# Performance work log

Hardware: AMD Instinct MI355X
Metric: run time of the kernel (lower is better)

Reference implementation:

```python
import jax, jax.numpy as jnp
import numpy as np

B, T, E, H = 2, 2048, 2048, 16
D = E // H  # head dim = 128
ROPE_BASE = 10000.0


def setup_inputs() -> dict:
    key = jax.random.key(0)
    ks = jax.random.split(key, 9)
    s = 1.0 / np.sqrt(E)
    return {
        "x": jax.random.normal(ks[0], (B, T, E), jnp.float32),
        "Wq": jax.random.normal(ks[1], (E, E), jnp.float32) * s,
        "bq": jax.random.normal(ks[2], (E,), jnp.float32) * s,
        "Wk": jax.random.normal(ks[3], (E, E), jnp.float32) * s,
        "bk": jax.random.normal(ks[4], (E,), jnp.float32) * s,
        "Wv": jax.random.normal(ks[5], (E, E), jnp.float32) * s,
        "bv": jax.random.normal(ks[6], (E,), jnp.float32) * s,
        "Wo": jax.random.normal(ks[7], (E, E), jnp.float32) * s,
        "bo": jax.random.normal(ks[8], (E,), jnp.float32) * s,
    }


def _rope(x):
    # x: [b, h, t, d]; positions are 1-indexed (m+1) as in the source
    t, d = x.shape[-2], x.shape[-1]
    j = jnp.arange(d // 2, dtype=x.dtype)
    thetas = ROPE_BASE ** (-2.0 * j / d)                  # [d/2]
    m = jnp.arange(1, t + 1, dtype=x.dtype)               # [t]
    ang = m[:, None] * thetas[None, :]                    # [t, d/2]
    C = jnp.concatenate([ang, ang], axis=-1)              # [t, d]
    x_rot = jnp.concatenate([-x[..., d // 2:], x[..., :d // 2]], axis=-1)
    return x * jnp.cos(C) + x_rot * jnp.sin(C)


def reference(x, Wq, bq, Wk, bk, Wv, bv, Wo, bo):
    b, t, e = x.shape
    # projections (nn.Linear: x @ W.T + b)
    def proj(W, bias):
        y = jnp.einsum('bte,fe->btf', x, W) + bias
        return y.reshape(b, t, H, D).transpose(0, 2, 1, 3)  # b h t d
    q = _rope(proj(Wq, bq))
    k = _rope(proj(Wk, bk))
    v = proj(Wv, bv)

    scale = jnp.sqrt(jnp.asarray(D, x.dtype))
    att = jnp.einsum('bhqd,bhkd->bhqk', q, k) / scale
    causal = jnp.tril(jnp.ones((t, t), bool))
    att = jnp.where(causal, att, -jnp.inf)
    att = jax.nn.softmax(att, axis=-1)
    y = jnp.einsum('bhqk,bhkd->bhqd', att, v)
    y = y.transpose(0, 2, 1, 3).reshape(b, t, e)
    y = jnp.einsum('bte,fe->btf', y, Wo) + bo
    return y
```

## Files before the change

### kernel.cpp

```cpp
#include <hip/hip_runtime.h>
#include <hip/hip_bf16.h>

typedef __bf16 bf16_t;
typedef __bf16 bf16x4 __attribute__((ext_vector_type(4)));
typedef __bf16 bf16x8 __attribute__((ext_vector_type(8)));
typedef float  f32x4  __attribute__((ext_vector_type(4)));

#define GLD_LDS16(gptr, lptr)                                                        \
    __builtin_amdgcn_global_load_lds((__attribute__((address_space(1))) void*)(gptr),\
                                     (__attribute__((address_space(3))) void*)(lptr),\
                                     16, 0, 0)

constexpr int Bc = 2, Tc = 2048, Ec = 2048, Hc = 16, Dc = 128;
constexpr int Mtok = Bc * Tc;

__device__ __forceinline__ bf16x8 cvt8(const float* p) {
    f32x4 a = *(const f32x4*)p;
    f32x4 b = *(const f32x4*)(p + 4);
    bf16x8 r;
    r[0] = (bf16_t)a[0]; r[1] = (bf16_t)a[1];
    r[2] = (bf16_t)a[2]; r[3] = (bf16_t)a[3];
    r[4] = (bf16_t)b[0]; r[5] = (bf16_t)b[1];
    r[6] = (bf16_t)b[2]; r[7] = (bf16_t)b[3];
    return r;
}

__global__ void convert_bf16(const float* __restrict__ src, bf16_t* __restrict__ dst) {
    size_t i = ((size_t)blockIdx.x * 256 + threadIdx.x) * 8;
    *(bf16x8*)&dst[i] = cvt8(src + i);
}

__global__ void convert_w(const float* __restrict__ Wq, const float* __restrict__ Wk,
                          const float* __restrict__ Wv, const float* __restrict__ Wo,
                          bf16_t* __restrict__ w4) {
    int blk = blockIdx.x;
    int wi  = blk >> 11;
    const float* src = (wi == 0) ? Wq : (wi == 1) ? Wk : (wi == 2) ? Wv : Wo;
    bf16_t* dst = w4 + (size_t)wi * Ec * Ec;
    size_t i = ((size_t)(blk & 2047) * 256 + threadIdx.x) * 8;
    *(bf16x8*)&dst[i] = cvt8(src + i);
}

__global__ __launch_bounds__(512, 2) void gemm_qkv_z(const bf16_t* __restrict__ A,
                                                     const bf16_t* __restrict__ w3,
                                                     const float* __restrict__ bq,
                                                     const float* __restrict__ bk,
                                                     const float* __restrict__ bv,
                                                     bf16_t* __restrict__ qo,
                                                     bf16_t* __restrict__ ko,
                                                     bf16_t* __restrict__ vto) {
    __shared__ __align__(16) bf16_t ldsA[3 * 8192];
    __shared__ __align__(16) bf16_t ldsB[3 * 12288];

    const int tid  = threadIdx.x;
    const int wave = tid >> 6;
    const int lane = tid & 63;
    const int g    = lane >> 4;
    const int n16  = lane & 15;
    const int wm   = wave >> 2;
    const int wn   = wave & 3;
    const int m0   = blockIdx.x * 256;
    const int n0   = blockIdx.y * 384;
    const int K    = Ec;

    const int sr   = tid >> 2;
    const int scol = (((tid & 3) ^ ((tid >> 3) & 3)) << 3);
    const bf16_t* srcA = A  + (size_t)(m0 + sr) * K + scol;
    const bf16_t* srcB = w3 + (size_t)(n0 + sr) * K + scol;
    const int dwave = wave * 512;

    const int fsw = (n16 >> 1) & 3;

    constexpr int NT = Ec / 32;

#define STG_A2(jj, buf)                                                         \
    do { if ((jj) < NT) {                                                       \
        const bf16_t* _s = srcA + (jj) * 32;                                    \
        bf16_t* _d = &ldsA[(buf) * 8192 + dwave];                               \
        GLD_LDS16(_s, _d);                                                      \
        GLD_LDS16(_s + (size_t)128 * K, _d + 4096);                             \
    } } while (0)
#define STG_B1(jj, buf)                                                         \
    do { if ((jj) < NT) {                                                       \
        GLD_LDS16(srcB + (jj) * 32, &ldsB[(buf) * 12288 + dwave]);              \
    } } while (0)
#define STG_B2(jj, buf)                                                         \
    do { if ((jj) < NT) {                                                       \
        const bf16_t* _s = srcB + (jj) * 32;                                    \
        bf16_t* _d = &ldsB[(buf) * 12288 + dwave];                              \
        GLD_LDS16(_s + (size_t)128 * K, _d + 4096);                             \
        GLD_LDS16(_s + (size_t)256 * K, _d + 8192);                             \
    } } while (0)

    f32x4 acc[8][6] = {};
    bf16x8 af[4], af2[4], bfr[6];

    STG_A2(0, 0); STG_B1(0, 0); STG_B2(0, 0);
    STG_A2(1, 1); STG_B1(1, 1); STG_B2(1, 1);
    asm volatile("s_waitcnt vmcnt(5)" ::: "memory");
    __builtin_amdgcn_s_barrier();
    asm volatile("" ::: "memory");

    int bc = 0;
    int bi = 2;
#pragma unroll 1
    for (int j = 0; j < NT; ++j) {
        const bf16_t* la = &ldsA[bc * 8192];
        const bf16_t* lb = &ldsB[bc * 12288];

#pragma unroll
        for (int mt = 0; mt < 4; ++mt)
            af[mt] = *(const bf16x8*)&la[(wm * 128 + mt * 16 + n16) * 32 +
                                         ((g ^ fsw) << 3)];
#pragma unroll
        for (int l = 0; l < 6; ++l)
            bfr[l] = *(const bf16x8*)&lb[(wn * 96 + l * 16 + n16) * 32 +
                                         ((g ^ fsw) << 3)];
        STG_A2(j + 2, bi);
        STG_B1(j + 2, bi);
        asm volatile("s_waitcnt lgkmcnt(0)" ::: "memory");
        __builtin_amdgcn_sched_barrier(0);
        __builtin_amdgcn_s_setprio(1);
#pragma unroll
        for (int mt = 0; mt < 4; ++mt)
#pragma unroll
            for (int l = 0; l < 6; ++l)
                acc[mt][l] = __builtin_amdgcn_mfma_f32_16x16x32_bf16(
                    af[mt], bfr[l], acc[mt][l], 0, 0, 0);
        __builtin_amdgcn_s_setprio(0);
        __builtin_amdgcn_s_barrier();
        asm volatile("" ::: "memory");

#pragma unroll
        for (int mt = 0; mt < 4; ++mt)
            af2[mt] = *(const bf16x8*)&la[(wm * 128 + 64 + mt * 16 + n16) * 32 +
                                          ((g ^ fsw) << 3)];
        STG_B2(j + 2, bi);
        asm volatile("s_waitcnt lgkmcnt(0)" ::: "memory");
        __builtin_amdgcn_sched_barrier(0);
        __builtin_amdgcn_s_setprio(1);
#pragma unroll
        for (int mt = 0; mt < 4; ++mt)
#pragma unroll
            for (int l = 0; l < 6; ++l)
                acc[4 + mt][l] = __builtin_amdgcn_mfma_f32_16x16x32_bf16(
                    af2[mt], bfr[l], acc[4 + mt][l], 0, 0, 0);
        __builtin_amdgcn_s_setprio(0);

        if (j < NT - 2)      { asm volatile("s_waitcnt vmcnt(5)" ::: "memory"); }
        else if (j < NT - 1) { asm volatile("s_waitcnt vmcnt(0)" ::: "memory"); }
        __builtin_amdgcn_s_barrier();
        asm volatile("" ::: "memory");

        bc = (bc == 2) ? 0 : bc + 1;
        bi = (bi == 2) ? 0 : bi + 1;
    }
#undef STG_A2
#undef STG_B1
#undef STG_B2

#pragma unroll
    for (int l = 0; l < 6; ++l) {
        int n   = n0 + wn * 96 + l * 16 + n16;
        int mat = n >> 11;
        int nn  = n & 2047;
        const float* bp = (mat == 0) ? bq : (mat == 1) ? bk : bv;
        float bn = bp[nn];
        int h = nn >> 7, d = nn & (Dc - 1);
#pragma unroll
        for (int i = 0; i < 8; ++i) {
            int mb = m0 + wm * 128 + (i >> 2) * 64 + (i & 3) * 16 + g * 4;
            int b = mb >> 11, t = mb & (Tc - 1);
            if (mat == 2) {
                bf16x4 pk;
#pragma unroll
                for (int r = 0; r < 4; ++r) pk[r] = (bf16_t)(acc[i][l][r] + bn);
                *(bf16x4*)&vto[(((size_t)(b * Hc + h)) * Dc + d) * Tc + t] = pk;
            } else {
                bf16_t* outb = (mat == 0) ? qo : ko;
#pragma unroll
                for (int r = 0; r < 4; ++r)
                    outb[(((size_t)(b * Hc + h)) * Tc + (t + r)) * Dc + d] =
                        (bf16_t)(acc[i][l][r] + bn);
            }
        }
    }
}

__global__ __launch_bounds__(512, 2) void gemm_out_p(const bf16_t* __restrict__ A,
                                                     const bf16_t* __restrict__ W,
                                                     const float* __restrict__ bias,
                                                     float* __restrict__ out) {
    __shared__ __align__(16) bf16_t ldsA[3 * 256 * 32];
    __shared__ __align__(16) bf16_t ldsB[3 * 128 * 32];

    const int tid  = threadIdx.x;
    const int wave = tid >> 6;
    const int lane = tid & 63;
    const int g    = lane >> 4;
    const int n16  = lane & 15;
    const int wm   = wave >> 1;
    const int wn   = wave & 1;
    const int m0   = blockIdx.x * 256;
    const int n0   = blockIdx.y * 128;
    const int K    = Ec;

    const int sr   = tid >> 2;
    const int scol = (((tid & 3) ^ ((tid >> 3) & 3)) << 3);
    const bf16_t* gA0 = A + (size_t)(m0 + sr) * K + scol;
    const bf16_t* gA1 = A + (size_t)(m0 + 128 + sr) * K + scol;
    const bf16_t* gB  = W + (size_t)(n0 + sr) * K + scol;
    const int dL = wave * 512;

    const int fsw = (n16 >> 1) & 3;
    const int rAo = (wm * 64 + n16) * 32 + ((g ^ fsw) << 3);
    const int rBo = (wn * 64 + n16) * 32 + ((g ^ fsw) << 3);

    f32x4 acc[4][4] = {};

    constexpr int NT = Ec / 32;
#pragma unroll
    for (int tt = 0; tt < 2; ++tt) {
        GLD_LDS16(gA0 + tt * 32, &ldsA[tt * 8192 + dL]);
        GLD_LDS16(gA1 + tt * 32, &ldsA[tt * 8192 + 4096 + dL]);
        GLD_LDS16(gB  + tt * 32, &ldsB[tt * 4096 + dL]);
    }

    int bc = 0, bi = 2;
#pragma unroll 1
    for (int t = 0; t < NT; ++t) {
        if (t < NT - 1) { asm volatile("s_waitcnt vmcnt(3)" ::: "memory"); }
        else            { asm volatile("s_waitcnt vmcnt(0)" ::: "memory"); }
        __builtin_amdgcn_s_barrier();
        asm volatile("" ::: "memory");

        const bf16_t* la = &ldsA[bc * 8192];
        const bf16_t* lb = &ldsB[bc * 4096];
        bf16x8 af[4], bfr[4];
#pragma unroll
        for (int mt = 0; mt < 4; ++mt) af[mt] = *(const bf16x8*)&la[rAo + mt * 512];
#pragma unroll
        for (int nt = 0; nt < 4; ++nt) bfr[nt] = *(const bf16x8*)&lb[rBo + nt * 512];

        if (t + 2 < NT) {
            GLD_LDS16(gA0 + (t + 2) * 32, &ldsA[bi * 8192 + dL]);
            GLD_LDS16(gA1 + (t + 2) * 32, &ldsA[bi * 8192 + 4096 + dL]);
            GLD_LDS16(gB  + (t + 2) * 32, &ldsB[bi * 4096 + dL]);
        }

        asm volatile("s_waitcnt lgkmcnt(0)" ::: "memory");
        __builtin_amdgcn_sched_barrier(0);
        __builtin_amdgcn_s_setprio(1);
#pragma unroll
        for (int mt = 0; mt < 4; ++mt)
#pragma unroll
            for (int nt = 0; nt < 4; ++nt)
                acc[mt][nt] = __builtin_amdgcn_mfma_f32_16x16x32_bf16(
                    af[mt], bfr[nt], acc[mt][nt], 0, 0, 0);
        __builtin_amdgcn_s_setprio(0);

        bc = (bc == 2) ? 0 : bc + 1;
        bi = (bi == 2) ? 0 : bi + 1;
    }

    const int row_off = wm * 64;
    const int col_off = wn * 64;
#pragma unroll
    for (int nt = 0; nt < 4; ++nt) {
        int n = n0 + col_off + nt * 16 + n16;
        float bn = bias[n];
#pragma unroll
        for (int mt = 0; mt < 4; ++mt) {
            int mb = m0 + row_off + mt * 16 + g * 4;
#pragma unroll
            for (int r = 0; r < 4; ++r)
                out[(size_t)(mb + r) * Ec + n] = acc[mt][nt][r] + bn;
        }
    }
}

__global__ __launch_bounds__(256) void gemm_qkv(const bf16_t* __restrict__ A,
                                                const float* __restrict__ Wq,
                                                const float* __restrict__ Wk,
                                                const float* __restrict__ Wv,
                                                const float* __restrict__ bq,
                                                const float* __restrict__ bk,
                                                const float* __restrict__ bv,
                                                bf16_t* __restrict__ qo,
                                                bf16_t* __restrict__ ko,
                                                bf16_t* __restrict__ vto) {
    __shared__ __align__(16) bf16_t ldsA[128 * 32];
    __shared__ __align__(16) bf16_t ldsB[128 * 32];

    const int tid  = threadIdx.x;
    const int wave = tid >> 6;
    const int lane = tid & 63;
    const int g    = lane >> 4;
    const int n16  = lane & 15;
    const int m0   = blockIdx.x * 128;
    const int mat  = blockIdx.y >> 4;
    const int n0   = (blockIdx.y & 15) * 128;
    const int row_off = (wave >> 1) * 64;
    const int col_off = (wave & 1) * 64;
    const int K = Ec;

    const float* W    = (mat == 0) ? Wq : (mat == 1) ? Wk : Wv;
    const float* bias = (mat == 0) ? bq : (mat == 1) ? bk : bv;

    f32x4 acc[4][4] = {};

    const int r0 = tid >> 2;
    const int cc = tid & 3;
    const size_t a0 = (size_t)(m0 + r0) * K + cc * 8;
    const size_t a1 = (size_t)(m0 + r0 + 64) * K + cc * 8;
    const float* pb0 = W + (size_t)(n0 + r0) * K + cc * 8;
    const float* pb1 = W + (size_t)(n0 + r0 + 64) * K + cc * 8;

    for (int k0 = 0; k0 < K; k0 += 32) {
        bf16x8 vb0 = cvt8(pb0 + k0);
        bf16x8 vb1 = cvt8(pb1 + k0);
        __syncthreads();
        GLD_LDS16(A + a0 + k0, &ldsA[(wave * 64) * 8]);
        GLD_LDS16(A + a1 + k0, &ldsA[(256 + wave * 64) * 8]);
        *(bf16x8*)&ldsB[(size_t)tid * 8]         = vb0;
        *(bf16x8*)&ldsB[(size_t)(256 + tid) * 8] = vb1;
        __syncthreads();

        bf16x8 af[4], bfr[4];
#pragma unroll
        for (int mt = 0; mt < 4; ++mt)
            af[mt] = *(const bf16x8*)&ldsA[(row_off + mt * 16 + n16) * 32 + g * 8];
#pragma unroll
        for (int nt = 0; nt < 4; ++nt)
            bfr[nt] = *(const bf16x8*)&ldsB[(col_off + nt * 16 + n16) * 32 + g * 8];
#pragma unroll
        for (int mt = 0; mt < 4; ++mt)
#pragma unroll
            for (int nt = 0; nt < 4; ++nt)
                acc[mt][nt] = __builtin_amdgcn_mfma_f32_16x16x32_bf16(
                    af[mt], bfr[nt], acc[mt][nt], 0, 0, 0);
    }

#pragma unroll
    for (int nt = 0; nt < 4; ++nt) {
        int n = n0 + col_off + nt * 16 + n16;
        float bn = bias[n];
        int h = n >> 7, d = n & (Dc - 1);
#pragma unroll
        for (int mt = 0; mt < 4; ++mt) {
            int mb = m0 + row_off + mt * 16 + g * 4;
            int b = mb >> 11, t = mb & (Tc - 1);
            if (mat == 2) {
                bf16x4 pk;
#pragma unroll
                for (int r = 0; r < 4; ++r) pk[r] = (bf16_t)(acc[mt][nt][r] + bn);
                *(bf16x4*)&vto[(((size_t)(b * Hc + h)) * Dc + d) * Tc + t] = pk;
            } else {
                bf16_t* outb = (mat == 0) ? qo : ko;
#pragma unroll
                for (int r = 0; r < 4; ++r)
                    outb[(((size_t)(b * Hc + h)) * Tc + (t + r)) * Dc + d] =
                        (bf16_t)(acc[mt][nt][r] + bn);
            }
        }
    }
}

__global__ __launch_bounds__(256) void gemm_out(const bf16_t* __restrict__ A,
                                                const float* __restrict__ W,
                                                const float* __restrict__ bias,
                                                float* __restrict__ out,
                                                int M, int N, int K) {
    __shared__ __align__(16) bf16_t ldsA[128 * 32];
    __shared__ __align__(16) bf16_t ldsB[128 * 32];

    const int tid  = threadIdx.x;
    const int wave = tid >> 6;
    const int lane = tid & 63;
    const int g    = lane >> 4;
    const int n16  = lane & 15;
    const int m0 = blockIdx.x * 128;
    const int n0 = blockIdx.y * 128;
    const int row_off = (wave >> 1) * 64;
    const int col_off = (wave & 1) * 64;

    f32x4 acc[4][4] = {};

    const int r0 = tid >> 2;
    const int cc = tid & 3;
    const size_t a0 = (size_t)(m0 + r0) * K + cc * 8;
    const size_t a1 = (size_t)(m0 + r0 + 64) * K + cc * 8;
    const float* pb0 = W + (size_t)(n0 + r0) * K + cc * 8;
    const float* pb1 = W + (size_t)(n0 + r0 + 64) * K + cc * 8;

    for (int k0 = 0; k0 < K; k0 += 32) {
        bf16x8 vb0 = cvt8(pb0 + k0);
        bf16x8 vb1 = cvt8(pb1 + k0);
        __syncthreads();
        GLD_LDS16(A + a0 + k0, &ldsA[(wave * 64) * 8]);
        GLD_LDS16(A + a1 + k0, &ldsA[(256 + wave * 64) * 8]);
        *(bf16x8*)&ldsB[(size_t)tid * 8]         = vb0;
        *(bf16x8*)&ldsB[(size_t)(256 + tid) * 8] = vb1;
        __syncthreads();

        bf16x8 af[4], bfr[4];
#pragma unroll
        for (int mt = 0; mt < 4; ++mt)
            af[mt] = *(const bf16x8*)&ldsA[(row_off + mt * 16 + n16) * 32 + g * 8];
#pragma unroll
        for (int nt = 0; nt < 4; ++nt)
            bfr[nt] = *(const bf16x8*)&ldsB[(col_off + nt * 16 + n16) * 32 + g * 8];
#pragma unroll
        for (int mt = 0; mt < 4; ++mt)
#pragma unroll
            for (int nt = 0; nt < 4; ++nt)
                acc[mt][nt] = __builtin_amdgcn_mfma_f32_16x16x32_bf16(
                    af[mt], bfr[nt], acc[mt][nt], 0, 0, 0);
    }

#pragma unroll
    for (int nt = 0; nt < 4; ++nt) {
        int n = n0 + col_off + nt * 16 + n16;
        float bn = bias[n];
#pragma unroll
        for (int mt = 0; mt < 4; ++mt) {
            int mb = m0 + row_off + mt * 16 + g * 4;
#pragma unroll
            for (int r = 0; r < 4; ++r)
                out[(size_t)(mb + r) * N + n] = acc[mt][nt][r] + bn;
        }
    }
}

__global__ void rope_kernel(bf16_t* __restrict__ q, bf16_t* __restrict__ k) {
    int row = blockIdx.x * 4 + (threadIdx.x >> 6);
    int d   = threadIdx.x & 63;
    int t   = row & (Tc - 1);
    const float sc2 = 0.08838834764831845f * 1.4426950408889634f;
    float theta = powf(10000.0f, -(float)d * (1.0f / 64.0f));
    float ang   = (float)(t + 1) * theta;
    float sv, cv;
    sincosf(ang, &sv, &cv);
    size_t base = (size_t)row * Dc;
    float q1 = (float)q[base + d], q2 = (float)q[base + d + 64];
    q[base + d]      = (bf16_t)((q1 * cv - q2 * sv) * sc2);
    q[base + d + 64] = (bf16_t)((q2 * cv + q1 * sv) * sc2);
    float k1 = (float)k[base + d], k2 = (float)k[base + d + 64];
    k[base + d]      = (bf16_t)(k1 * cv - k2 * sv);
    k[base + d + 64] = (bf16_t)(k2 * cv + k1 * sv);
}

constexpr int KP = 128 + 8;
constexpr int VP = 64 + 8;
constexpr int PP = 64 + 8;

__global__ __launch_bounds__(256, 3) void attn_kernel(const bf16_t* __restrict__ q,
                                                      const bf16_t* __restrict__ kmat,
                                                      const bf16_t* __restrict__ vt,
                                                      bf16_t* __restrict__ out) {
    __shared__ __align__(16) bf16_t k_lds[64 * KP];
    __shared__ __align__(16) bf16_t v_lds[128 * VP];
    __shared__ __align__(16) bf16_t p_lds[4 * 16 * PP];

    const int tid  = threadIdx.x;
    const int wave = tid >> 6, lane = tid & 63;
    const int g = lane >> 4, n16 = lane & 15;
    const int pi = blockIdx.x;
    const int bh = blockIdx.y;
    const size_t base = (size_t)bh * Tc * Dc;
    const int b = bh >> 4, h = bh & 15;
    bf16_t* pw = &p_lds[wave * 16 * PP];

    const int kr_key = tid >> 4, kr_c = tid & 15;
    const int vr_dd  = tid >> 3, vr_c = tid & 7;

#pragma unroll 1
    for (int half = 0; half < 2; ++half) {
        const int qt = half ? pi : 31 - pi;
        const int q0 = qt * 64;

        bf16x8 qf[4];
        {
            const bf16_t* qp = q + base + (size_t)(q0 + wave * 16 + n16) * Dc + g * 8;
#pragma unroll
            for (int kk = 0; kk < 4; ++kk) qf[kk] = *(const bf16x8*)(qp + kk * 32);
        }

        float m_run[4], l_run[4];
#pragma unroll
        for (int r = 0; r < 4; ++r) { m_run[r] = -1e30f; l_run[r] = 0.0f; }
        f32x4 o_acc[8] = {};

        bf16x8 rk[4], rv[4];
#pragma unroll
        for (int i = 0; i < 4; ++i)
            rk[i] = *(const bf16x8*)&kmat[base + (size_t)(i * 16 + kr_key) * Dc + kr_c * 8];
#pragma unroll
        for (int i = 0; i < 4; ++i)
            rv[i] = *(const bf16x8*)&vt[base + (size_t)(i * 32 + vr_dd) * Tc + vr_c * 8];

#pragma unroll 1
        for (int kt = 0; kt <= qt; ++kt) {
            const int k0 = kt * 64;
            __syncthreads();
#pragma unroll
            for (int i = 0; i < 4; ++i)
                *(bf16x8*)&k_lds[(i * 16 + kr_key) * KP + kr_c * 8] = rk[i];
#pragma unroll
            for (int i = 0; i < 4; ++i)
                *(bf16x8*)&v_lds[(i * 32 + vr_dd) * VP + vr_c * 8] = rv[i];
            __syncthreads();

            if (kt < qt) {
                const int kn = k0 + 64;
#pragma unroll
                for (int i = 0; i < 4; ++i)
                    rk[i] = *(const bf16x8*)&kmat[base + (size_t)(kn + i * 16 + kr_key) * Dc + kr_c * 8];
#pragma unroll
                for (int i = 0; i < 4; ++i)
                    rv[i] = *(const bf16x8*)&vt[base + (size_t)(i * 32 + vr_dd) * Tc + kn + vr_c * 8];
            }

            f32x4 s_acc[4];
#pragma unroll
            for (int nt = 0; nt < 4; ++nt) {
                f32x4 a = {};
                int key = nt * 16 + n16;
#pragma unroll
                for (int kk = 0; kk < 4; ++kk) {
                    bf16x8 kf = *(const bf16x8*)&k_lds[key * KP + kk * 32 + g * 8];
                    a = __builtin_amdgcn_mfma_f32_16x16x32_bf16(qf[kk], kf, a, 0, 0, 0);
                }
                s_acc[nt] = a;
            }

            if (kt == qt) {
#pragma unroll
                for (int nt = 0; nt < 4; ++nt) {
                    int key = k0 + nt * 16 + n16;
#pragma unroll
                    for (int r = 0; r < 4; ++r) {
                        int qq = q0 + wave * 16 + g * 4 + r;
                        if (key > qq) s_acc[nt][r] = -1e30f;
                    }
                }
            }

            float rm4[4];
            int ok = 1;
#pragma unroll
            for (int r = 0; r < 4; ++r) {
                float rm = fmaxf(fmaxf(s_acc[0][r], s_acc[1][r]),
                                 fmaxf(s_acc[2][r], s_acc[3][r]));
                rm = fmaxf(rm, __shfl_xor(rm, 1, 16));
                rm = fmaxf(rm, __shfl_xor(rm, 2, 16));
                rm = fmaxf(rm, __shfl_xor(rm, 4, 16));
                rm = fmaxf(rm, __shfl_xor(rm, 8, 16));
                rm4[r] = rm;
                ok &= (rm <= m_run[r] + 8.0f);
            }
            if (__all(ok)) {
#pragma unroll
                for (int r = 0; r < 4; ++r) {
                    float sum = 0.0f;
#pragma unroll
                    for (int nt = 0; nt < 4; ++nt) {
                        float p = __builtin_amdgcn_exp2f(s_acc[nt][r] - m_run[r]);
                        s_acc[nt][r] = p;
                        sum += p;
                    }
                    l_run[r] += sum;
                }
            } else {
                float alpha[4];
#pragma unroll
                for (int r = 0; r < 4; ++r) {
                    float m_new = fmaxf(m_run[r], rm4[r]);
                    alpha[r] = __builtin_amdgcn_exp2f(m_run[r] - m_new);
                    m_run[r] = m_new;
                    float sum = 0.0f;
#pragma unroll
                    for (int nt = 0; nt < 4; ++nt) {
                        float p = __builtin_amdgcn_exp2f(s_acc[nt][r] - m_new);
                        s_acc[nt][r] = p;
                        sum += p;
                    }
                    l_run[r] = l_run[r] * alpha[r] + sum;
                }
#pragma unroll
                for (int dt = 0; dt < 8; ++dt)
#pragma unroll
                    for (int r = 0; r < 4; ++r) o_acc[dt][r] *= alpha[r];
            }

#pragma unroll
            for (int nt = 0; nt < 4; ++nt) {
                int key = nt * 16 + n16;
#pragma unroll
                for (int r = 0; r < 4; ++r)
                    pw[(g * 4 + r) * PP + key] = (bf16_t)s_acc[nt][r];
            }
            bf16x8 pf[2];
#pragma unroll
            for (int kk = 0; kk < 2; ++kk)
                pf[kk] = *(const bf16x8*)&pw[n16 * PP + kk * 32 + g * 8];

#pragma unroll
            for (int dt = 0; dt < 8; ++dt) {
                int dd = dt * 16 + n16;
#pragma unroll
                for (int kk = 0; kk < 2; ++kk) {
                    bf16x8 vf = *(const bf16x8*)&v_lds[dd * VP + kk * 32 + g * 8];
                    o_acc[dt] = __builtin_amdgcn_mfma_f32_16x16x32_bf16(
                        pf[kk], vf, o_acc[dt], 0, 0, 0);
                }
            }
        }

        float inv_l[4];
#pragma unroll
        for (int r = 0; r < 4; ++r) {
            float s = l_run[r];
            s += __shfl_xor(s, 1, 16);
            s += __shfl_xor(s, 2, 16);
            s += __shfl_xor(s, 4, 16);
            s += __shfl_xor(s, 8, 16);
            inv_l[r] = 1.0f / s;
        }
#pragma unroll
        for (int dt = 0; dt < 8; ++dt) {
            int d = dt * 16 + n16;
#pragma unroll
            for (int r = 0; r < 4; ++r) {
                int qq = q0 + wave * 16 + g * 4 + r;
                out[((size_t)(b * Tc + qq)) * Ec + h * Dc + d] =
                    (bf16_t)(o_acc[dt][r] * inv_l[r]);
            }
        }
    }
}

extern "C" void kernel_launch(void* const* d_in, const int* in_sizes, int n_in,
                              void* d_out, int out_size, void* d_ws, size_t ws_size,
                              hipStream_t stream) {
    const float* x  = (const float*)d_in[0];
    const float* Wq = (const float*)d_in[1];
    const float* bq = (const float*)d_in[2];
    const float* Wk = (const float*)d_in[3];
    const float* bk = (const float*)d_in[4];
    const float* Wv = (const float*)d_in[5];
    const float* bv = (const float*)d_in[6];
    const float* Wo = (const float*)d_in[7];
    const float* bo = (const float*)d_in[8];
    float* out = (float*)d_out;

    char* ws = (char*)d_ws;
    const size_t sz  = (size_t)Bc * Hc * Tc * Dc * sizeof(bf16_t);
    const size_t szW = (size_t)Ec * Ec * sizeof(bf16_t);
    bf16_t* q   = (bf16_t*)(ws);
    bf16_t* k   = (bf16_t*)(ws + sz);
    bf16_t* vt  = (bf16_t*)(ws + 2 * sz);
    bf16_t* xb  = (bf16_t*)(ws + 3 * sz);
    bf16_t* att = xb;

    if (ws_size >= 4 * sz + 4 * szW) {
        bf16_t* w4 = (bf16_t*)(ws + 4 * sz);
        convert_bf16<<<Mtok * Ec / (256 * 8), 256, 0, stream>>>(x, xb);
        convert_w<<<8192, 256, 0, stream>>>(Wq, Wk, Wv, Wo, w4);
        gemm_qkv_z<<<dim3(Mtok / 256, 16), 512, 0, stream>>>(xb, w4, bq, bk, bv,
                                                             q, k, vt);
        rope_kernel<<<Bc * Hc * Tc / 4, 256, 0, stream>>>(q, k);
        attn_kernel<<<dim3(16, Bc * Hc), 256, 0, stream>>>(q, k, vt, att);
        gemm_out_p<<<dim3(Mtok / 256, Ec / 128), 512, 0, stream>>>(
            att, w4 + 3 * (size_t)Ec * Ec, bo, out);
    } else {
        convert_bf16<<<Mtok * Ec / (256 * 8), 256, 0, stream>>>(x, xb);
        gemm_qkv<<<dim3(Mtok / 128, 48), 256, 0, stream>>>(xb, Wq, Wk, Wv,
                                                           bq, bk, bv, q, k, vt);
        rope_kernel<<<Bc * Hc * Tc / 4, 256, 0, stream>>>(q, k);
        attn_kernel<<<dim3(16, Bc * Hc), 256, 0, stream>>>(q, k, vt, att);
        gemm_out<<<dim3(Mtok / 128, Ec / 128), 256, 0, stream>>>(att, Wo, bo, out,
                                                                 Mtok, Ec, Ec);
    }
}
```

Before: 462.8 us.

## Swizzle attention K/V LDS tiles with XOR and remap grid for head locality

Replaces the padded K and V shared-memory tiles with unpadded tiles whose 16-byte chunks are XOR-swizzled by row, which cuts LDS footprint and is meant to avoid bank conflicts on the MFMA operand reads. The 2D grid becomes a 1D grid of 512 blocks, remapped so that groups of 8 consecutive blocks cover different heads at the same query-tile pair, aiming for better scheduling and cache locality. The occupancy hint of 3 blocks per CU is removed from launch_bounds, so the compiler may now use more registers. Any mismatch between the write and read swizzle patterns would corrupt results.

Measured after the change: 442.8 us. -4.3%, faster.

```diff
diff --git a/kernel.cpp b/kernel.cpp
--- a/kernel.cpp
+++ b/kernel.cpp
@@ -450,29 +450,31 @@
     k[base + d + 64] = (bf16_t)(k2 * cv + k1 * sv);
 }
 
-constexpr int KP = 128 + 8;
-constexpr int VP = 64 + 8;
 constexpr int PP = 64 + 8;
 
-__global__ __launch_bounds__(256, 3) void attn_kernel(const bf16_t* __restrict__ q,
-                                                      const bf16_t* __restrict__ kmat,
-                                                      const bf16_t* __restrict__ vt,
-                                                      bf16_t* __restrict__ out) {
-    __shared__ __align__(16) bf16_t k_lds[64 * KP];
-    __shared__ __align__(16) bf16_t v_lds[128 * VP];
+__global__ __launch_bounds__(256) void attn_kernel(const bf16_t* __restrict__ q,
+                                                   const bf16_t* __restrict__ kmat,
+                                                   const bf16_t* __restrict__ vt,
+                                                   bf16_t* __restrict__ out) {
+    __shared__ __align__(16) bf16_t k_lds[64 * 128];
+    __shared__ __align__(16) bf16_t v_lds[128 * 64];
     __shared__ __align__(16) bf16_t p_lds[4 * 16 * PP];
 
     const int tid  = threadIdx.x;
     const int wave = tid >> 6, lane = tid & 63;
     const int g = lane >> 4, n16 = lane & 15;
-    const int pi = blockIdx.x;
-    const int bh = blockIdx.y;
+    const int id = blockIdx.x;
+    const int pi = (id >> 3) & 15;
+    const int bh = (id & 7) + ((id >> 7) << 3);
     const size_t base = (size_t)bh * Tc * Dc;
     const int b = bh >> 4, h = bh & 15;
     bf16_t* pw = &p_lds[wave * 16 * PP];
 
     const int kr_key = tid >> 4, kr_c = tid & 15;
     const int vr_dd  = tid >> 3, vr_c = tid & 7;
+    const int kwx = (kr_key & 7) << 3;
+    const int vwx = (vr_dd & 7) << 3;
+    const int rxo = (n16 & 7) << 3;
 
 #pragma unroll 1
     for (int half = 0; half < 2; ++half) {
@@ -505,10 +507,10 @@
             __syncthreads();
 #pragma unroll
             for (int i = 0; i < 4; ++i)
-                *(bf16x8*)&k_lds[(i * 16 + kr_key) * KP + kr_c * 8] = rk[i];
+                *(bf16x8*)&k_lds[(i * 16 + kr_key) * 128 + ((kr_c * 8) ^ kwx)] = rk[i];
 #pragma unroll
             for (int i = 0; i < 4; ++i)
-                *(bf16x8*)&v_lds[(i * 32 + vr_dd) * VP + vr_c * 8] = rv[i];
+                *(bf16x8*)&v_lds[(i * 32 + vr_dd) * 64 + ((vr_c * 8) ^ vwx)] = rv[i];
             __syncthreads();
 
             if (kt < qt) {
@@ -528,7 +530,8 @@
                 int key = nt * 16 + n16;
 #pragma unroll
                 for (int kk = 0; kk < 4; ++kk) {
-                    bf16x8 kf = *(const bf16x8*)&k_lds[key * KP + kk * 32 + g * 8];
+                    bf16x8 kf = *(const bf16x8*)
+                        &k_lds[key * 128 + ((kk * 32 + g * 8) ^ rxo)];
                     a = __builtin_amdgcn_mfma_f32_16x16x32_bf16(qf[kk], kf, a, 0, 0, 0);
                 }
                 s_acc[nt] = a;
@@ -610,7 +613,8 @@
                 int dd = dt * 16 + n16;
 #pragma unroll
                 for (int kk = 0; kk < 2; ++kk) {
-                    bf16x8 vf = *(const bf16x8*)&v_lds[dd * VP + kk * 32 + g * 8];
+                    bf16x8 vf = *(const bf16x8*)
+                        &v_lds[dd * 64 + ((kk * 32 + g * 8) ^ rxo)];
                     o_acc[dt] = __builtin_amdgcn_mfma_f32_16x16x32_bf16(
                         pf[kk], vf, o_acc[dt], 0, 0, 0);
                 }
@@ -670,7 +674,7 @@
         gemm_qkv_z<<<dim3(Mtok / 256, 16), 512, 0, stream>>>(xb, w4, bq, bk, bv,
                                                              q, k, vt);
         rope_kernel<<<Bc * Hc * Tc / 4, 256, 0, stream>>>(q, k);
-        attn_kernel<<<dim3(16, Bc * Hc), 256, 0, stream>>>(q, k, vt, att);
+        attn_kernel<<<dim3(512), 256, 0, stream>>>(q, k, vt, att);
         gemm_out_p<<<dim3(Mtok / 256, Ec / 128), 512, 0, stream>>>(
             att, w4 + 3 * (size_t)Ec * Ec, bo, out);
     } else {
@@ -678,7 +682,7 @@
         gemm_qkv<<<dim3(Mtok / 128, 48), 256, 0, stream>>>(xb, Wq, Wk, Wv,
                                                            bq, bk, bv, q, k, vt);
         rope_kernel<<<Bc * Hc * Tc / 4, 256, 0, stream>>>(q, k);
-        attn_kernel<<<dim3(16, Bc * Hc), 256, 0, stream>>>(q, k, vt, att);
+        attn_kernel<<<dim3(512), 256, 0, stream>>>(q, k, vt, att);
         gemm_out<<<dim3(Mtok / 128, Ec / 128), 256, 0, stream>>>(att, Wo, bo, out,
                                                                  Mtok, Ec, Ec);
     }
```
